# Kernel tuning notes

Measured on AMD Instinct MI355X. Metric: run time of the kernel, lower is better.

## Reference

```python
import jax, jax.numpy as jnp
import numpy as np

T, D, E = 65536, 1024, 64  # tokens, d_model, n_experts

def setup_inputs() -> dict:
    key = jax.random.key(0)
    k1, k2 = jax.random.split(key)
    x = jax.random.normal(k1, (T, D), dtype=jnp.float32)
    Wg = jax.random.normal(k2, (D, E), dtype=jnp.float32) * (1.0 / np.sqrt(D))
    return {"x": x, "Wg": Wg, "top_k": 2}

def reference(x, Wg, top_k):
    # Token-to-expert gating: logits -> softmax -> top-k -> renormalized combine weights.
    logits = jnp.einsum('td,de->te', x, Wg)            # [T, E]
    probs = jax.nn.softmax(logits, axis=-1)            # [T, E]
    topk_vals, topk_idx = jax.lax.top_k(probs, top_k)  # [T, k], [T, k]
    combine = topk_vals / jnp.sum(topk_vals, axis=-1, keepdims=True)  # renormalize over selected experts
    return combine, topk_idx, probs
```

## Files before the change

kernel.cpp:

```cpp
#include <hip/hip_runtime.h>
#include <math.h>


#define D_DIM 1024
#define E_DIM 64
#define TPB   256
#define TOK   128
#define DC    16
#define NCH   (D_DIM / DC)
#define XS    20
#define LS    65

__global__ __launch_bounds__(TPB, 2) void router_kernel(
    const float* __restrict__ x, const float* __restrict__ Wg,
    float* __restrict__ out, int T)
{
    __shared__ float smem[8448];
    float* const sx = smem;
    float* const sw = smem + 5120;

    const int tid  = threadIdx.x;
    const int eg   = tid & 15;
    const int TG   = tid >> 4;
    const int e0   = eg << 2;
    const int base = blockIdx.x * TOK;

    float acc[8][4];
#pragma unroll
    for (int i = 0; i < 8; ++i)
#pragma unroll
        for (int j = 0; j < 4; ++j) acc[i][j] = 0.0f;

    const int xr0 = tid >> 2;
    const int xc0 = (tid & 3) << 2;
    const float* __restrict__ xg0 = x + (size_t)(base + xr0) * D_DIM + xc0;
    const float* __restrict__ xg1 = xg0 + (size_t)64 * D_DIM;
    const int wd0 = tid >> 4;
    const int wc0 = (tid & 15) << 2;
    const float* __restrict__ wg0 = Wg + (size_t)wd0 * E_DIM + wc0;

    float4 xs0, xs1, wsr;

    xs0 = *(const float4*)xg0;
    xs1 = *(const float4*)xg1;
    wsr = *(const float4*)wg0;
    *(float4*)&sx[xr0 * XS + xc0]        = xs0;
    *(float4*)&sx[(xr0 + 64) * XS + xc0] = xs1;
    *(float4*)&sw[wd0 * E_DIM + wc0]     = wsr;
    xs0 = *(const float4*)(xg0 + DC);
    xs1 = *(const float4*)(xg1 + DC);
    wsr = *(const float4*)(wg0 + (size_t)DC * E_DIM);
    __syncthreads();

    for (int ch = 0; ch < NCH; ++ch) {
        const int cur = ch & 1;
        if (ch + 1 < NCH) {
            float* const dx = sx + (cur ^ 1) * (TOK * XS);
            float* const dw = sw + (cur ^ 1) * (DC * E_DIM);
            *(float4*)&dx[xr0 * XS + xc0]        = xs0;
            *(float4*)&dx[(xr0 + 64) * XS + xc0] = xs1;
            *(float4*)&dw[wd0 * E_DIM + wc0]     = wsr;
        }
        if (ch + 2 < NCH) {
            xs0 = *(const float4*)(xg0 + (ch + 2) * DC);
            xs1 = *(const float4*)(xg1 + (ch + 2) * DC);
            wsr = *(const float4*)(wg0 + (size_t)(ch + 2) * DC * E_DIM);
        }

        const float* __restrict__ bx = sx + cur * (TOK * XS);
        const float* __restrict__ bw = sw + cur * (DC * E_DIM);

#pragma unroll
        for (int g = 0; g < DC; g += 4) {
            const float4 w0 = *(const float4*)&bw[(g + 0) * E_DIM + e0];
            const float4 w1 = *(const float4*)&bw[(g + 1) * E_DIM + e0];
            const float4 w2 = *(const float4*)&bw[(g + 2) * E_DIM + e0];
            const float4 w3 = *(const float4*)&bw[(g + 3) * E_DIM + e0];
#pragma unroll
            for (int i = 0; i < 8; ++i) {
                const float4 xv = *(const float4*)&bx[(TG + 16 * i) * XS + g];
                acc[i][0] = fmaf(xv.x, w0.x, acc[i][0]);
                acc[i][0] = fmaf(xv.y, w1.x, acc[i][0]);
                acc[i][0] = fmaf(xv.z, w2.x, acc[i][0]);
                acc[i][0] = fmaf(xv.w, w3.x, acc[i][0]);
                acc[i][1] = fmaf(xv.x, w0.y, acc[i][1]);
                acc[i][1] = fmaf(xv.y, w1.y, acc[i][1]);
                acc[i][1] = fmaf(xv.z, w2.y, acc[i][1]);
                acc[i][1] = fmaf(xv.w, w3.y, acc[i][1]);
                acc[i][2] = fmaf(xv.x, w0.z, acc[i][2]);
                acc[i][2] = fmaf(xv.y, w1.z, acc[i][2]);
                acc[i][2] = fmaf(xv.z, w2.z, acc[i][2]);
                acc[i][2] = fmaf(xv.w, w3.z, acc[i][2]);
                acc[i][3] = fmaf(xv.x, w0.w, acc[i][3]);
                acc[i][3] = fmaf(xv.y, w1.w, acc[i][3]);
                acc[i][3] = fmaf(xv.z, w2.w, acc[i][3]);
                acc[i][3] = fmaf(xv.w, w3.w, acc[i][3]);
            }
        }
        __syncthreads();
    }

    float* const sl = smem;
#pragma unroll
    for (int i = 0; i < 8; ++i) {
        const int row = (TG + 16 * i) * LS + e0;
        sl[row + 0] = acc[i][0];
        sl[row + 1] = acc[i][1];
        sl[row + 2] = acc[i][2];
        sl[row + 3] = acc[i][3];
    }
    __syncthreads();

    if (tid < TOK) {
        const int t = tid;
        float m = -INFINITY;
#pragma unroll
        for (int e = 0; e < E_DIM; ++e) m = fmaxf(m, sl[t * LS + e]);

        float s = 0.0f;
#pragma unroll
        for (int e = 0; e < E_DIM; ++e) {
            const float p = expf(sl[t * LS + e] - m);
            sl[t * LS + e] = p;
            s += p;
        }
        const float inv = 1.0f / s;

        float v1 = -1.0f, v2 = -1.0f;
        int   i1 = 0,     i2 = 0;
#pragma unroll
        for (int e = 0; e < E_DIM; ++e) {
            const float p = sl[t * LS + e] * inv;
            sl[t * LS + e] = p;
            if (p > v1)      { v2 = v1; i2 = i1; v1 = p; i1 = e; }
            else if (p > v2) { v2 = p;  i2 = e; }
        }

        const float denom = v1 + v2;
        const int token = base + t;
        *(float2*)&out[(size_t)2 * token]                 = make_float2(v1 / denom, v2 / denom);
        *(float2*)&out[(size_t)2 * T + (size_t)2 * token] = make_float2((float)i1, (float)i2);
    }
    __syncthreads();

    float* __restrict__ po = out + (size_t)4 * T + (size_t)base * E_DIM;
#pragma unroll
    for (int k = 0; k < 8; ++k) {
        const int g = (tid + k * TPB) << 2;
        const int t = g >> 6;
        const int e = g & 63;
        *(float4*)&po[g] = make_float4(sl[t * LS + e],     sl[t * LS + e + 1],
                                       sl[t * LS + e + 2], sl[t * LS + e + 3]);
    }
}

extern "C" void kernel_launch(void* const* d_in, const int* in_sizes, int n_in,
                              void* d_out, int out_size, void* d_ws, size_t ws_size,
                              hipStream_t stream) {
    const float* x  = (const float*)d_in[0];
    const float* Wg = (const float*)d_in[1];
    float* out = (float*)d_out;
    const int T = in_sizes[0] / D_DIM;

    router_kernel<<<dim3(T / TOK), dim3(TPB), 0, stream>>>(x, Wg, out, T);
}
```

Baseline: 407.2 us.

## Use split-bf16 MFMA for gating matmul with fp64 repair of near-tie tokens

Replaces the scalar FP32 FMA matmul with bf16 MFMA instructions. Both x and Wg are split into hi and lo bf16 parts and three products are summed to approximate FP32 accuracy. Wg is pre-swizzled by a small prep kernel, and softmax and top-2 selection are computed in registers with cross-lane shuffles. Tokens whose top-3 logits fall within a margin are queued and recomputed in double precision by a repair kernel, so index selection stays correct. The cost is two extra launches, atomics, and results that hold only up to the chosen margin.

```diff
diff --git a/kernel.cpp b/kernel.cpp
--- a/kernel.cpp
+++ b/kernel.cpp
@@ -4,163 +4,304 @@
 
 #define D_DIM 1024
 #define E_DIM 64
+#define TM    128
+#define KC    64
+#define NCH   (D_DIM / KC)
 #define TPB   256
-#define TOK   128
-#define DC    16
-#define NCH   (D_DIM / DC)
-#define XS    20
-#define LS    65
-
-__global__ __launch_bounds__(TPB, 2) void router_kernel(
+#define MARGIN 1e-3f
+#define WT_U4  16384
+
+typedef float f32x4 __attribute__((ext_vector_type(4)));
+typedef short s16x8 __attribute__((ext_vector_type(8)));
+
+__device__ __forceinline__ unsigned bf16hi_rne(unsigned u) {
+  return (u + 0x7FFFu + ((u >> 16) & 1u)) & 0xFFFF0000u;
+}
+
+__global__ void wprep_kernel(const float* __restrict__ Wg, uint4* __restrict__ w4,
+                             unsigned* __restrict__ ctr) {
+  const int gi = blockIdx.x * blockDim.x + threadIdx.x;
+  if (gi == 0) ctr[0] = 0u;
+  const int ch = gi >> 9;
+  const int e  = (gi >> 3) & 63;
+  const int g  = gi & 7;
+  const int k0 = ch * KC + (g ^ (e & 7)) * 8;
+  unsigned hp[4], lp[4];
+#pragma unroll
+  for (int jj = 0; jj < 4; ++jj) {
+    const float w0 = Wg[(k0 + 2 * jj    ) * E_DIM + e];
+    const float w1 = Wg[(k0 + 2 * jj + 1) * E_DIM + e];
+    const unsigned h0 = bf16hi_rne(__float_as_uint(w0));
+    const unsigned h1 = bf16hi_rne(__float_as_uint(w1));
+    const float l0 = w0 - __uint_as_float(h0);
+    const float l1 = w1 - __uint_as_float(h1);
+    hp[jj] = h1 | (h0 >> 16);
+    lp[jj] = bf16hi_rne(__float_as_uint(l1)) | (bf16hi_rne(__float_as_uint(l0)) >> 16);
+  }
+  w4[gi]         = make_uint4(hp[0], hp[1], hp[2], hp[3]);
+  w4[8192 + gi]  = make_uint4(lp[0], lp[1], lp[2], lp[3]);
+}
+
+struct Frag2 { s16x8 hi, lo; };
+
+__device__ __forceinline__ Frag2 cvt8(const float4 a, const float4 b) {
+  const float f[8] = {a.x, a.y, a.z, a.w, b.x, b.y, b.z, b.w};
+  unsigned h[8], l[8];
+#pragma unroll
+  for (int i = 0; i < 8; ++i) {
+    const unsigned hb = bf16hi_rne(__float_as_uint(f[i]));
+    const float lf = f[i] - __uint_as_float(hb);
+    h[i] = hb;
+    l[i] = bf16hi_rne(__float_as_uint(lf));
+  }
+  union { uint4 u; s16x8 v; } H, L;
+  H.u = make_uint4(h[1] | (h[0] >> 16), h[3] | (h[2] >> 16),
+                   h[5] | (h[4] >> 16), h[7] | (h[6] >> 16));
+  L.u = make_uint4(l[1] | (l[0] >> 16), l[3] | (l[2] >> 16),
+                   l[5] | (l[4] >> 16), l[7] | (l[6] >> 16));
+  Frag2 r; r.hi = H.v; r.lo = L.v; return r;
+}
+
+__global__ __launch_bounds__(TPB, 2) void router_mfma(
+    const float* __restrict__ x, const uint4* __restrict__ wt,
+    float* __restrict__ out, unsigned* __restrict__ ctr,
+    unsigned* __restrict__ list, int rcap, int T)
+{
+  __shared__ uint4 sw[2][1024];
+
+  const int tid   = threadIdx.x;
+  const int wid   = tid >> 6;
+  const int lane  = tid & 63;
+  const int c     = lane & 15;
+  const int q     = lane >> 4;
+  const int twave = blockIdx.x * TM + wid * 32;
+
+  f32x4 acc[4][2];
+#pragma unroll
+  for (int et = 0; et < 4; ++et)
+#pragma unroll
+    for (int tt = 0; tt < 2; ++tt)
+      acc[et][tt] = (f32x4){0.f, 0.f, 0.f, 0.f};
+
+  const float* xb0 = x + (size_t)(twave + c) * D_DIM + q * 8;
+  const float* xb1 = xb0 + (size_t)16 * D_DIM;
+
+  uint4  wr[4];
+  float4 xr[8];
+
+#pragma unroll
+  for (int i = 0; i < 4; ++i) wr[i] = wt[(i >> 1) * 8192 + (i & 1) * 256 + tid];
+#pragma unroll
+  for (int i = 0; i < 4; ++i) sw[0][(i >> 1) * 512 + (i & 1) * 256 + tid] = wr[i];
+#pragma unroll
+  for (int v = 0; v < 8; ++v) {
+    const int tt = v >> 2, s = (v >> 1) & 1, h = v & 1;
+    const float* b = (tt ? xb1 : xb0);
+    xr[v] = *(const float4*)(b + s * 32 + h * 4);
+  }
+#pragma unroll
+  for (int i = 0; i < 4; ++i) wr[i] = wt[(i >> 1) * 8192 + 512 + (i & 1) * 256 + tid];
+  __syncthreads();
+
+  const int row0 = c * 64;
+  const int g0 = ((0 + q) ^ (c & 7)) * 8;
+  const int g1 = ((4 + q) ^ (c & 7)) * 8;
+
+  for (int ch = 0; ch < NCH; ++ch) {
+    const int cur = ch & 1;
+    if (ch + 1 < NCH) {
+#pragma unroll
+      for (int i = 0; i < 4; ++i)
+        sw[cur ^ 1][(i >> 1) * 512 + (i & 1) * 256 + tid] = wr[i];
+    }
+    if (ch + 2 < NCH) {
+#pragma unroll
+      for (int i = 0; i < 4; ++i)
+        wr[i] = wt[(i >> 1) * 8192 + (ch + 2) * 512 + (i & 1) * 256 + tid];
+    }
+
+    Frag2 bx[2][2];
+#pragma unroll
+    for (int tt = 0; tt < 2; ++tt)
+#pragma unroll
+      for (int s = 0; s < 2; ++s)
+        bx[tt][s] = cvt8(xr[tt * 4 + s * 2 + 0], xr[tt * 4 + s * 2 + 1]);
+
+    if (ch + 1 < NCH) {
+#pragma unroll
+      for (int v = 0; v < 8; ++v) {
+        const int tt = v >> 2, s = (v >> 1) & 1, h = v & 1;
+        const float* b = (tt ? xb1 : xb0);
+        xr[v] = *(const float4*)(b + (ch + 1) * KC + s * 32 + h * 4);
+      }
+    }
+
+    const ushort* bufh = (const ushort*)&sw[cur][0];
+    const ushort* bufl = bufh + 4096;
+#pragma unroll
+    for (int s = 0; s < 2; ++s) {
+      const int go = s ? g1 : g0;
+      s16x8 ah[4], al[4];
+#pragma unroll
+      for (int et = 0; et < 4; ++et) {
+        ah[et] = *(const s16x8*)(bufh + et * 1024 + row0 + go);
+        al[et] = *(const s16x8*)(bufl + et * 1024 + row0 + go);
+      }
+#pragma unroll
+      for (int et = 0; et < 4; ++et)
+#pragma unroll
+        for (int tt = 0; tt < 2; ++tt) {
+          f32x4 a = acc[et][tt];
+          a = __builtin_amdgcn_mfma_f32_16x16x32_bf16(ah[et], bx[tt][s].hi, a, 0, 0, 0);
+          a = __builtin_amdgcn_mfma_f32_16x16x32_bf16(ah[et], bx[tt][s].lo, a, 0, 0, 0);
+          a = __builtin_amdgcn_mfma_f32_16x16x32_bf16(al[et], bx[tt][s].hi, a, 0, 0, 0);
+          acc[et][tt] = a;
+        }
+    }
+    __syncthreads();
+  }
+
+  const size_t Ts = (size_t)T;
+  float* const comb = out;
+  float* const idxo = out + 2 * Ts;
+  float* const prob = out + 4 * Ts;
+
+#pragma unroll
+  for (int tt = 0; tt < 2; ++tt) {
+    const int tok = twave + tt * 16 + c;
+    float v[16];
+#pragma unroll
+    for (int et = 0; et < 4; ++et)
+#pragma unroll
+      for (int r = 0; r < 4; ++r) v[et * 4 + r] = acc[et][tt][r];
+
+    float v1 = v[0], v2 = -INFINITY, v3 = -INFINITY;
+    int   i1 = q * 4, i2 = 0;
+#pragma unroll
+    for (int et = 0; et < 4; ++et)
+#pragma unroll
+      for (int r = 0; r < 4; ++r) {
+        if (et == 0 && r == 0) continue;
+        const float p  = v[et * 4 + r];
+        const int   ei = et * 16 + q * 4 + r;
+        if (p > v1)      { v3 = v2; v2 = v1; i2 = i1; v1 = p; i1 = ei; }
+        else if (p > v2) { v3 = v2; v2 = p;  i2 = ei; }
+        else if (p > v3) { v3 = p; }
+      }
+#pragma unroll
+    for (int d = 16; d <= 32; d <<= 1) {
+      const float ov1 = __shfl_xor(v1, d); const int oi1 = __shfl_xor(i1, d);
+      const float ov2 = __shfl_xor(v2, d); const int oi2 = __shfl_xor(i2, d);
+      const float ov3 = __shfl_xor(v3, d);
+      const bool  ob1 = (ov1 > v1) || (ov1 == v1 && oi1 < i1);
+      const float w1v = ob1 ? ov1 : v1;  const int w1i = ob1 ? oi1 : i1;
+      const float l1v = ob1 ? v1  : ov1; const int l1i = ob1 ? i1  : oi1;
+      const float w2v = ob1 ? ov2 : v2;  const int w2i = ob1 ? oi2 : i2;
+      const float ls2 = ob1 ? v2  : ov2;
+      const float ws3 = ob1 ? ov3 : v3;
+      const bool  b2  = (l1v > w2v) || (l1v == w2v && l1i < w2i);
+      const float a2v = b2 ? l1v : w2v; const int a2i = b2 ? l1i : w2i;
+      const float a3v = b2 ? fmaxf(w2v, ls2) : fmaxf(l1v, ws3);
+      v1 = w1v; i1 = w1i; v2 = a2v; i2 = a2i; v3 = a3v;
+    }
+
+    float s = 0.f;
+#pragma unroll
+    for (int i = 0; i < 16; ++i) { v[i] = __expf(v[i] - v1); s += v[i]; }
+    s += __shfl_xor(s, 16);
+    s += __shfl_xor(s, 32);
+    const float inv = 1.f / s;
+
+#pragma unroll
+    for (int et = 0; et < 4; ++et)
+      *(float4*)&prob[(size_t)tok * E_DIM + et * 16 + q * 4] =
+          make_float4(v[et * 4 + 0] * inv, v[et * 4 + 1] * inv,
+                      v[et * 4 + 2] * inv, v[et * 4 + 3] * inv);
+
+    if (q == 0) {
+      if ((v1 - v2 < MARGIN) || (v2 - v3 < MARGIN)) {
+        const unsigned slot = atomicAdd(ctr, 1u);
+        if ((int)slot < rcap) list[slot] = (unsigned)tok;
+      }
+      const float c1 = 1.f / (1.f + __expf(v2 - v1));
+      *(float2*)&comb[2 * (size_t)tok] = make_float2(c1, 1.f - c1);
+      *(float2*)&idxo[2 * (size_t)tok] = make_float2((float)i1, (float)i2);
+    }
+  }
+}
+
+__global__ __launch_bounds__(256) void repair_kernel(
     const float* __restrict__ x, const float* __restrict__ Wg,
-    float* __restrict__ out, int T)
+    float* __restrict__ out, const unsigned* __restrict__ ctr,
+    const unsigned* __restrict__ list, int rcap, int T)
 {
-    __shared__ float smem[8448];
-    float* const sx = smem;
-    float* const sw = smem + 5120;
-
-    const int tid  = threadIdx.x;
-    const int eg   = tid & 15;
-    const int TG   = tid >> 4;
-    const int e0   = eg << 2;
-    const int base = blockIdx.x * TOK;
-
-    float acc[8][4];
-#pragma unroll
-    for (int i = 0; i < 8; ++i)
-#pragma unroll
-        for (int j = 0; j < 4; ++j) acc[i][j] = 0.0f;
-
-    const int xr0 = tid >> 2;
-    const int xc0 = (tid & 3) << 2;
-    const float* __restrict__ xg0 = x + (size_t)(base + xr0) * D_DIM + xc0;
-    const float* __restrict__ xg1 = xg0 + (size_t)64 * D_DIM;
-    const int wd0 = tid >> 4;
-    const int wc0 = (tid & 15) << 2;
-    const float* __restrict__ wg0 = Wg + (size_t)wd0 * E_DIM + wc0;
-
-    float4 xs0, xs1, wsr;
-
-    xs0 = *(const float4*)xg0;
-    xs1 = *(const float4*)xg1;
-    wsr = *(const float4*)wg0;
-    *(float4*)&sx[xr0 * XS + xc0]        = xs0;
-    *(float4*)&sx[(xr0 + 64) * XS + xc0] = xs1;
-    *(float4*)&sw[wd0 * E_DIM + wc0]     = wsr;
-    xs0 = *(const float4*)(xg0 + DC);
-    xs1 = *(const float4*)(xg1 + DC);
-    wsr = *(const float4*)(wg0 + (size_t)DC * E_DIM);
+  __shared__ double part[4][E_DIM];
+  const int tid = threadIdx.x;
+  const int e   = tid & 63;
+  const int s   = tid >> 6;
+  const unsigned total = ctr[0];
+  const unsigned n = total < (unsigned)rcap ? total : (unsigned)rcap;
+
+  for (unsigned j = blockIdx.x; j < n; j += gridDim.x) {
+    const int t = (int)list[j];
+    const float* xr = x  + (size_t)t * D_DIM + s * 256;
+    const float* wr = Wg + (size_t)(s * 256) * E_DIM + e;
+    double a = 0.0;
+#pragma unroll 8
+    for (int d = 0; d < 256; ++d)
+      a += (double)xr[d] * (double)wr[(size_t)d * E_DIM];
+    part[s][e] = a;
     __syncthreads();
-
-    for (int ch = 0; ch < NCH; ++ch) {
-        const int cur = ch & 1;
-        if (ch + 1 < NCH) {
-            float* const dx = sx + (cur ^ 1) * (TOK * XS);
-            float* const dw = sw + (cur ^ 1) * (DC * E_DIM);
-            *(float4*)&dx[xr0 * XS + xc0]        = xs0;
-            *(float4*)&dx[(xr0 + 64) * XS + xc0] = xs1;
-            *(float4*)&dw[wd0 * E_DIM + wc0]     = wsr;
-        }
-        if (ch + 2 < NCH) {
-            xs0 = *(const float4*)(xg0 + (ch + 2) * DC);
-            xs1 = *(const float4*)(xg1 + (ch + 2) * DC);
-            wsr = *(const float4*)(wg0 + (size_t)(ch + 2) * DC * E_DIM);
-        }
-
-        const float* __restrict__ bx = sx + cur * (TOK * XS);
-        const float* __restrict__ bw = sw + cur * (DC * E_DIM);
-
-#pragma unroll
-        for (int g = 0; g < DC; g += 4) {
-            const float4 w0 = *(const float4*)&bw[(g + 0) * E_DIM + e0];
-            const float4 w1 = *(const float4*)&bw[(g + 1) * E_DIM + e0];
-            const float4 w2 = *(const float4*)&bw[(g + 2) * E_DIM + e0];
-            const float4 w3 = *(const float4*)&bw[(g + 3) * E_DIM + e0];
-#pragma unroll
-            for (int i = 0; i < 8; ++i) {
-                const float4 xv = *(const float4*)&bx[(TG + 16 * i) * XS + g];
-                acc[i][0] = fmaf(xv.x, w0.x, acc[i][0]);
-                acc[i][0] = fmaf(xv.y, w1.x, acc[i][0]);
-                acc[i][0] = fmaf(xv.z, w2.x, acc[i][0]);
-                acc[i][0] = fmaf(xv.w, w3.x, acc[i][0]);
-                acc[i][1] = fmaf(xv.x, w0.y, acc[i][1]);
-                acc[i][1] = fmaf(xv.y, w1.y, acc[i][1]);
-                acc[i][1] = fmaf(xv.z, w2.y, acc[i][1]);
-                acc[i][1] = fmaf(xv.w, w3.y, acc[i][1]);
-                acc[i][2] = fmaf(xv.x, w0.z, acc[i][2]);
-                acc[i][2] = fmaf(xv.y, w1.z, acc[i][2]);
-                acc[i][2] = fmaf(xv.z, w2.z, acc[i][2]);
-                acc[i][2] = fmaf(xv.w, w3.z, acc[i][2]);
-                acc[i][3] = fmaf(xv.x, w0.w, acc[i][3]);
-                acc[i][3] = fmaf(xv.y, w1.w, acc[i][3]);
-                acc[i][3] = fmaf(xv.z, w2.w, acc[i][3]);
-                acc[i][3] = fmaf(xv.w, w3.w, acc[i][3]);
-            }
-        }
-        __syncthreads();
-    }
-
-    float* const sl = smem;
-#pragma unroll
-    for (int i = 0; i < 8; ++i) {
-        const int row = (TG + 16 * i) * LS + e0;
-        sl[row + 0] = acc[i][0];
-        sl[row + 1] = acc[i][1];
-        sl[row + 2] = acc[i][2];
-        sl[row + 3] = acc[i][3];
+    if (tid < 64) {
+      const float l = (float)(part[0][e] + part[1][e] + part[2][e] + part[3][e]);
+      float m = l;
+#pragma unroll
+      for (int d2 = 1; d2 < 64; d2 <<= 1) m = fmaxf(m, __shfl_xor(m, d2));
+      const float p = expf(l - m);
+      float ss = p;
+#pragma unroll
+      for (int d2 = 1; d2 < 64; d2 <<= 1) ss += __shfl_xor(ss, d2);
+      out[4 * (size_t)T + (size_t)t * E_DIM + e] = p / ss;
+      float v1 = l, v2 = -INFINITY; int i1 = e, i2 = 0;
+#pragma unroll
+      for (int d2 = 1; d2 < 64; d2 <<= 1) {
+        const float ov1 = __shfl_xor(v1, d2); const int oi1 = __shfl_xor(i1, d2);
+        const float ov2 = __shfl_xor(v2, d2); const int oi2 = __shfl_xor(i2, d2);
+        const bool  ob1 = (ov1 > v1) || (ov1 == v1 && oi1 < i1);
+        const float w1v = ob1 ? ov1 : v1;  const int w1i = ob1 ? oi1 : i1;
+        const float l1v = ob1 ? v1  : ov1; const int l1i = ob1 ? i1  : oi1;
+        const float w2v = ob1 ? ov2 : v2;  const int w2i = ob1 ? oi2 : i2;
+        const bool  b2  = (l1v > w2v) || (l1v == w2v && l1i < w2i);
+        v1 = w1v; i1 = w1i;
+        v2 = b2 ? l1v : w2v; i2 = b2 ? l1i : w2i;
+      }
+      if (e == 0) {
+        const float c1 = 1.f / (1.f + expf(v2 - v1));
+        out[2 * (size_t)t]     = c1;
+        out[2 * (size_t)t + 1] = 1.f - c1;
+        out[2 * (size_t)T + 2 * (size_t)t]     = (float)i1;
+        out[2 * (size_t)T + 2 * (size_t)t + 1] = (float)i2;
+      }
     }
     __syncthreads();
-
-    if (tid < TOK) {
-        const int t = tid;
-        float m = -INFINITY;
-#pragma unroll
-        for (int e = 0; e < E_DIM; ++e) m = fmaxf(m, sl[t * LS + e]);
-
-        float s = 0.0f;
-#pragma unroll
-        for (int e = 0; e < E_DIM; ++e) {
-            const float p = expf(sl[t * LS + e] - m);
-            sl[t * LS + e] = p;
-            s += p;
-        }
-        const float inv = 1.0f / s;
-
-        float v1 = -1.0f, v2 = -1.0f;
-        int   i1 = 0,     i2 = 0;
-#pragma unroll
-        for (int e = 0; e < E_DIM; ++e) {
-            const float p = sl[t * LS + e] * inv;
-            sl[t * LS + e] = p;
-            if (p > v1)      { v2 = v1; i2 = i1; v1 = p; i1 = e; }
-            else if (p > v2) { v2 = p;  i2 = e; }
-        }
-
-        const float denom = v1 + v2;
-        const int token = base + t;
-        *(float2*)&out[(size_t)2 * token]                 = make_float2(v1 / denom, v2 / denom);
-        *(float2*)&out[(size_t)2 * T + (size_t)2 * token] = make_float2((float)i1, (float)i2);
-    }
-    __syncthreads();
-
-    float* __restrict__ po = out + (size_t)4 * T + (size_t)base * E_DIM;
-#pragma unroll
-    for (int k = 0; k < 8; ++k) {
-        const int g = (tid + k * TPB) << 2;
-        const int t = g >> 6;
-        const int e = g & 63;
-        *(float4*)&po[g] = make_float4(sl[t * LS + e],     sl[t * LS + e + 1],
-                                       sl[t * LS + e + 2], sl[t * LS + e + 3]);
-    }
+  }
 }
 
 extern "C" void kernel_launch(void* const* d_in, const int* in_sizes, int n_in,
                               void* d_out, int out_size, void* d_ws, size_t ws_size,
                               hipStream_t stream) {
-    const float* x  = (const float*)d_in[0];
-    const float* Wg = (const float*)d_in[1];
-    float* out = (float*)d_out;
-    const int T = in_sizes[0] / D_DIM;
-
-    router_kernel<<<dim3(T / TOK), dim3(TPB), 0, stream>>>(x, Wg, out, T);
-}
+  const float* x  = (const float*)d_in[0];
+  const float* Wg = (const float*)d_in[1];
+  float* out = (float*)d_out;
+  uint4* wt  = (uint4*)d_ws;
+  unsigned* ctr  = (unsigned*)d_ws + WT_U4 * 4;
+  unsigned* list = ctr + 1;
+  const int T = in_sizes[0] / D_DIM;
+
+  long avail = ((long)ws_size - (long)(WT_U4 * 16 + 4)) / 4;
+  int rcap = avail < 0 ? 0 : (avail > 8192 ? 8192 : (int)avail);
+
+  wprep_kernel<<<dim3(NCH * E_DIM * 8 / TPB), dim3(TPB), 0, stream>>>(Wg, wt, ctr);
+  router_mfma<<<dim3(T / TM), dim3(TPB), 0, stream>>>(x, wt, out, ctr, list, rcap, T);
+  repair_kernel<<<dim3(1024), dim3(256), 0, stream>>>(x, Wg, out, ctr, list, rcap, T);
+}
```

Result: slower. 420.4 us (+3.2%).
